# Optimization experiments

Measured on AMD Instinct MI355X. Metric: run time of the kernel, lower is better.

Reference implementation:

```python
import jax, jax.numpy as jnp
import numpy as np

NUM_LAYERS = 16
ALPHA = 1.0
EPS = 1e-20

def setup_inputs() -> dict:
    key = jax.random.key(0)
    k1, k2, k3, k4 = jax.random.split(key, 4)
    B, S, M, G = 8, 9, 8, 512
    M2 = M * M
    return {
        "dict_real": jax.random.normal(k1, (B, S, M2, G), dtype=jnp.float32),
        "dict_imag": jax.random.normal(k2, (B, S, M2, G), dtype=jnp.float32),
        "cov_real": jax.random.normal(k3, (B, S, M, M), dtype=jnp.float32),
        "cov_imag": jax.random.normal(k4, (B, S, M, M), dtype=jnp.float32),
    }

def reference(dict_real, dict_imag, cov_real, cov_imag):
    D = (dict_real + 1j * dict_imag).astype(jnp.complex64)   # (B,S,M2,G) dictionary_band
    C = (cov_real + 1j * cov_imag).astype(jnp.complex64)     # (B,S,M,M) covariance matrix
    B, S, M, _ = C.shape
    G = D.shape[-1]
    # covariance_vector = cov.transpose(2,3).reshape(B,S,M2,1)
    r = jnp.swapaxes(C, 2, 3).reshape(B, S, M * M, 1)
    Dh = jnp.conj(jnp.swapaxes(D, 2, 3))                     # (B,S,G,M2)
    DhD = jnp.matmul(Dh, D)                                  # (B,S,G,G) Hermitian PSD
    Dhr = jnp.matmul(Dh, r)                                  # (B,S,G,1)
    # initial spectrum: real part, L2-normalized over grid dim
    res = jnp.real(Dhr).astype(jnp.float32)
    res = res / (jnp.linalg.norm(res, axis=2, keepdims=True) + EPS)
    # gamma = 1 / max|eig(D^H D)|; Hermitian PSD so eigvalsh gives same max magnitude
    eig = jnp.linalg.eigvalsh(DhD)                           # (B,S,G) real
    gamma = 1.0 / jnp.max(jnp.abs(eig), axis=2, keepdims=True)        # (B,S,1)
    lam = 0.5 * jnp.max(jnp.abs(Dhr), axis=2, keepdims=True).reshape(B, S, 1)
    theta = (ALPHA * lam * gamma).reshape(B, S, 1, 1)
    g = gamma.reshape(B, S, 1, 1).astype(jnp.complex64)
    I = jnp.eye(G, dtype=jnp.complex64)
    Wt = I - g * DhD                                         # (B,S,G,G)
    Wer = g * Dhr                                            # We @ r, constant per layer

    def step(res_c, _):
        s = jnp.matmul(Wt, res_c.astype(jnp.complex64)) + Wer
        res_new = jax.nn.relu(jnp.abs(s) - theta)            # soft-shrinkage on magnitude
        return res_new, res_new

    res_final, res_all = jax.lax.scan(step, res, None, length=NUM_LAYERS)
    result_init_all = jnp.moveaxis(res_all, 0, 2)            # (B,S,L,G,1)

    def minmax_norm(x):
        lo = jnp.min(x, axis=2, keepdims=True)
        hi = jnp.max(x, axis=2, keepdims=True)
        return (x - lo) / (hi - lo + EPS)

    result_ave = minmax_norm(jnp.mean(res_final, axis=1, keepdims=True).astype(jnp.float32))
    result = minmax_norm(res_final)
    return (result, result_ave, result_init_all)
```

## Files before the change

### kernel.cpp

```cpp
#include <hip/hip_runtime.h>
#include <math.h>

#define N_SQ   7
#define INV_P  (1.0f / 256.0f)
#define EPS_F  1e-20f
#define PH     72
#define PQ     67
#define PLANE  (64 * PH)

typedef _Float16 h2    __attribute__((ext_vector_type(2)));
typedef _Float16 f16x8 __attribute__((ext_vector_type(8)));
typedef float    f32x4 __attribute__((ext_vector_type(4)));

__device__ inline float cdot2(h2 a, h2 b, float c) {
#if __has_builtin(__builtin_amdgcn_fdot2)
    return __builtin_amdgcn_fdot2(a, b, c, false);
#else
    return c + (float)a.x * (float)b.x + (float)a.y * (float)b.y;
#endif
}
__device__ inline h2 bch2(unsigned int x) { return __builtin_bit_cast(h2, x); }
__device__ inline h2 bch2f(float x)       { return __builtin_bit_cast(h2, x); }
__device__ inline float bcf(h2 x)         { return __builtin_bit_cast(float, x); }


__global__ __launch_bounds__(512, 1) void ista_main_kernel(
    const float* __restrict__ Dre, const float* __restrict__ Dim,
    const float* __restrict__ Cre, const float* __restrict__ Cim,
    float* __restrict__ out, float* __restrict__ ws)
{
    const int bs = blockIdx.x;
    const int t  = threadIdx.x;
    const int wv = t >> 6;
    const int ln = t & 63;
    const int c16 = ln & 15;
    const int qd  = ln >> 4;
    const float* __restrict__ dre = Dre + (size_t)bs * 32768;
    const float* __restrict__ dim = Dim + (size_t)bs * 32768;

    __shared__ __align__(16) float uBuf[12800];
    _Float16* ShRe  = (_Float16*)uBuf;
    _Float16* ShIm  = (_Float16*)uBuf + PLANE;
    float*    Q1    = uBuf + 4608;
    float*    resHist = uBuf + 4608;
    _Float16* sResH = (_Float16*)(uBuf + 2048);
    __shared__ __align__(16) float s_r[128];
    __shared__ float s_red[32];

    if (t < 64) {
        int i = t >> 3, j = t & 7;
        s_r[2 * t]     = Cre[bs * 64 + j * 8 + i];
        s_r[2 * t + 1] = Cim[bs * 64 + j * 8 + i];
    }

    const int tau0 = 2 * wv, tau1 = 2 * wv + 1;
    const int I0 = tau0 >> 2, J0 = tau0 & 3;
    const int I1 = tau1 >> 2, J1 = tau1 & 3;

    float Elog = 0.f, gamma = 0.f;

    auto epilogue = [&](f32x4 P0, f32x4 Qa0, f32x4 P1, f32x4 Qa1, bool first, bool last) {
        #pragma unroll
        for (int r = 0; r < 4; ++r) {
            Q1[(I0 * 16 + qd * 4 + r) * PQ + J0 * 16 + c16] = Qa0[r];
            Q1[(I1 * 16 + qd * 4 + r) * PQ + J1 * 16 + c16] = Qa1[r];
        }
        float dv = 0.f;
        if (I0 == J0) {
            #pragma unroll
            for (int r = 0; r < 4; ++r) if (qd * 4 + r == c16) dv = fmaxf(dv, fabsf(P0[r]));
        }
        if (I1 == J1) {
            #pragma unroll
            for (int r = 0; r < 4; ++r) if (qd * 4 + r == c16) dv = fmaxf(dv, fabsf(P1[r]));
        }
        for (int off = 32; off; off >>= 1) dv = fmaxf(dv, __shfl_down(dv, off, 64));
        if (ln == 0) s_red[wv] = dv;
        __syncthreads();
        float m = s_red[0];
        #pragma unroll
        for (int k = 1; k < 8; ++k) m = fmaxf(m, s_red[k]);
        Elog = first ? log2f(m) : 2.f * Elog + log2f(m);
        float ic = 1.f / m;
        float ci0[4], ci1[4];
        #pragma unroll
        for (int r = 0; r < 4; ++r) {
            ci0[r] = Qa0[r] - Q1[(J0 * 16 + c16) * PQ + I0 * 16 + qd * 4 + r];
            ci1[r] = Qa1[r] - Q1[(J1 * 16 + c16) * PQ + I1 * 16 + qd * 4 + r];
        }
        if (!last) {
            #pragma unroll
            for (int r = 0; r < 4; ++r) {
                ShRe[(I0 * 16 + qd * 4 + r) * PH + J0 * 16 + c16] = (_Float16)(P0[r] * ic);
                ShIm[(I0 * 16 + qd * 4 + r) * PH + J0 * 16 + c16] = (_Float16)(ci0[r] * ic);
                ShRe[(I1 * 16 + qd * 4 + r) * PH + J1 * 16 + c16] = (_Float16)(P1[r] * ic);
                ShIm[(I1 * 16 + qd * 4 + r) * PH + J1 * 16 + c16] = (_Float16)(ci1[r] * ic);
            }
            __syncthreads();
        } else {
            float fr = 0.f;
            #pragma unroll
            for (int r = 0; r < 4; ++r)
                fr += P0[r] * P0[r] + ci0[r] * ci0[r] + P1[r] * P1[r] + ci1[r] * ci1[r];
            fr *= ic * ic;
            for (int off = 32; off; off >>= 1) fr += __shfl_down(fr, off, 64);
            if (ln == 0) s_red[8 + wv] = fr;
            __syncthreads();
            float fsum = 0.f;
            #pragma unroll
            for (int k = 0; k < 8; ++k) fsum += s_red[8 + k];
            gamma = exp2f(-(2.f * Elog + log2f(fsum)) * INV_P);
        }
    };

    h2 du_re[32], du_im[32];
    f32x4 gP0 = {0.f, 0.f, 0.f, 0.f}, gQ0 = {0.f, 0.f, 0.f, 0.f};
    f32x4 gP1 = {0.f, 0.f, 0.f, 0.f}, gQ1 = {0.f, 0.f, 0.f, 0.f};
    {
        const int srow = t >> 4;
        const int scb  = (t & 15) * 4;
        float4 pr0, pi0, pr1, pi1;
        pr0 = *(const float4*)&dre[srow * 512 + scb];
        pi0 = *(const float4*)&dim[srow * 512 + scb];
        pr1 = *(const float4*)&dre[(srow + 32) * 512 + scb];
        pi1 = *(const float4*)&dim[(srow + 32) * 512 + scb];
        for (int ch = 0; ch < 8; ++ch) {
            *(h2*)&ShRe[srow * PH + scb]     = h2{(_Float16)pr0.x, (_Float16)pr0.y};
            *(h2*)&ShRe[srow * PH + scb + 2] = h2{(_Float16)pr0.z, (_Float16)pr0.w};
            *(h2*)&ShIm[srow * PH + scb]     = h2{(_Float16)pi0.x, (_Float16)pi0.y};
            *(h2*)&ShIm[srow * PH + scb + 2] = h2{(_Float16)pi0.z, (_Float16)pi0.w};
            *(h2*)&ShRe[(srow + 32) * PH + scb]     = h2{(_Float16)pr1.x, (_Float16)pr1.y};
            *(h2*)&ShRe[(srow + 32) * PH + scb + 2] = h2{(_Float16)pr1.z, (_Float16)pr1.w};
            *(h2*)&ShIm[(srow + 32) * PH + scb]     = h2{(_Float16)pi1.x, (_Float16)pi1.y};
            *(h2*)&ShIm[(srow + 32) * PH + scb + 2] = h2{(_Float16)pi1.z, (_Float16)pi1.w};
            if (ch < 7) {
                int gc = (ch + 1) * 64;
                pr0 = *(const float4*)&dre[srow * 512 + gc + scb];
                pi0 = *(const float4*)&dim[srow * 512 + gc + scb];
                pr1 = *(const float4*)&dre[(srow + 32) * 512 + gc + scb];
                pi1 = *(const float4*)&dim[(srow + 32) * 512 + gc + scb];
            }
            __syncthreads();
            #pragma unroll
            for (int ks = 0; ks < 64; ks += 32) {
                f16x8 arI0 = *(const f16x8*)&ShRe[(I0 * 16 + c16) * PH + ks + qd * 8];
                f16x8 aiI0 = *(const f16x8*)&ShIm[(I0 * 16 + c16) * PH + ks + qd * 8];
                f16x8 arJ0 = *(const f16x8*)&ShRe[(J0 * 16 + c16) * PH + ks + qd * 8];
                f16x8 aiJ0 = *(const f16x8*)&ShIm[(J0 * 16 + c16) * PH + ks + qd * 8];
                gP0 = __builtin_amdgcn_mfma_f32_16x16x32_f16(arI0, arJ0, gP0, 0, 0, 0);
                gP0 = __builtin_amdgcn_mfma_f32_16x16x32_f16(aiI0, aiJ0, gP0, 0, 0, 0);
                gQ0 = __builtin_amdgcn_mfma_f32_16x16x32_f16(aiI0, arJ0, gQ0, 0, 0, 0);
                f16x8 arI1 = *(const f16x8*)&ShRe[(I1 * 16 + c16) * PH + ks + qd * 8];
                f16x8 aiI1 = *(const f16x8*)&ShIm[(I1 * 16 + c16) * PH + ks + qd * 8];
                f16x8 arJ1 = *(const f16x8*)&ShRe[(J1 * 16 + c16) * PH + ks + qd * 8];
                f16x8 aiJ1 = *(const f16x8*)&ShIm[(J1 * 16 + c16) * PH + ks + qd * 8];
                gP1 = __builtin_amdgcn_mfma_f32_16x16x32_f16(arI1, arJ1, gP1, 0, 0, 0);
                gP1 = __builtin_amdgcn_mfma_f32_16x16x32_f16(aiI1, aiJ1, gP1, 0, 0, 0);
                gQ1 = __builtin_amdgcn_mfma_f32_16x16x32_f16(aiI1, arJ1, gQ1, 0, 0, 0);
            }
            if (ch == wv) {
                #pragma unroll
                for (int c = 0; c < 8; ++c) {
                    uint4 aw = *(const uint4*)&ShRe[ln * PH + 8 * c];
                    du_re[4 * c + 0] = bch2(aw.x); du_re[4 * c + 1] = bch2(aw.y);
                    du_re[4 * c + 2] = bch2(aw.z); du_re[4 * c + 3] = bch2(aw.w);
                    uint4 bw = *(const uint4*)&ShIm[ln * PH + 8 * c];
                    du_im[4 * c + 0] = bch2(bw.x); du_im[4 * c + 1] = bch2(bw.y);
                    du_im[4 * c + 2] = bch2(bw.z); du_im[4 * c + 3] = bch2(bw.w);
                }
            }
            __syncthreads();
        }
    }
    epilogue(gP0, gQ0, gP1, gQ1, true, false);

    for (int sq = 0; sq < N_SQ; ++sq) {
        f32x4 P0 = {0.f, 0.f, 0.f, 0.f}, Qa0 = {0.f, 0.f, 0.f, 0.f};
        f32x4 P1 = {0.f, 0.f, 0.f, 0.f}, Qa1 = {0.f, 0.f, 0.f, 0.f};
        #pragma unroll
        for (int ks = 0; ks < 64; ks += 32) {
            f16x8 arI0 = *(const f16x8*)&ShRe[(I0 * 16 + c16) * PH + ks + qd * 8];
            f16x8 aiI0 = *(const f16x8*)&ShIm[(I0 * 16 + c16) * PH + ks + qd * 8];
            f16x8 arJ0 = *(const f16x8*)&ShRe[(J0 * 16 + c16) * PH + ks + qd * 8];
            f16x8 aiJ0 = *(const f16x8*)&ShIm[(J0 * 16 + c16) * PH + ks + qd * 8];
            P0  = __builtin_amdgcn_mfma_f32_16x16x32_f16(arI0, arJ0, P0, 0, 0, 0);
            P0  = __builtin_amdgcn_mfma_f32_16x16x32_f16(aiI0, aiJ0, P0, 0, 0, 0);
            Qa0 = __builtin_amdgcn_mfma_f32_16x16x32_f16(aiI0, arJ0, Qa0, 0, 0, 0);
            f16x8 arI1 = *(const f16x8*)&ShRe[(I1 * 16 + c16) * PH + ks + qd * 8];
            f16x8 aiI1 = *(const f16x8*)&ShIm[(I1 * 16 + c16) * PH + ks + qd * 8];
            f16x8 arJ1 = *(const f16x8*)&ShRe[(J1 * 16 + c16) * PH + ks + qd * 8];
            f16x8 aiJ1 = *(const f16x8*)&ShIm[(J1 * 16 + c16) * PH + ks + qd * 8];
            P1  = __builtin_amdgcn_mfma_f32_16x16x32_f16(arI1, arJ1, P1, 0, 0, 0);
            P1  = __builtin_amdgcn_mfma_f32_16x16x32_f16(aiI1, aiJ1, P1, 0, 0, 0);
            Qa1 = __builtin_amdgcn_mfma_f32_16x16x32_f16(aiI1, arJ1, Qa1, 0, 0, 0);
        }
        epilogue(P0, Qa0, P1, Qa1, false, sq == N_SQ - 1);
    }

    float dhr_re, dhr_im, res_g, theta;
    h2 dV[64];
    {
        float dr0 = 0.f, dr1 = 0.f, di0 = 0.f, di1 = 0.f;
        #pragma unroll
        for (int m = 0; m < 64; ++m) {
            float ar = dre[m * 512 + t], ai = dim[m * 512 + t];
            dV[m] = h2{(_Float16)ar, (_Float16)ai};
            float rr = s_r[2 * m], ri = s_r[2 * m + 1];
            if (m & 1) { dr1 += ar * rr + ai * ri; di1 += ar * ri - ai * rr; }
            else       { dr0 += ar * rr + ai * ri; di0 += ar * ri - ai * rr; }
        }
        dhr_re = dr0 + dr1; dhr_im = di0 + di1;
        float sv = dhr_re * dhr_re;
        float mv = sqrtf(dhr_re * dhr_re + dhr_im * dhr_im);
        for (int off = 32; off; off >>= 1) {
            sv += __shfl_down(sv, off, 64);
            mv = fmaxf(mv, __shfl_down(mv, off, 64));
        }
        if (ln == 0) { s_red[16 + wv] = sv; s_red[24 + wv] = mv; }
        __syncthreads();
        float ss = 0.f, mmx = 0.f;
        #pragma unroll
        for (int k = 0; k < 8; ++k) { ss += s_red[16 + k]; mmx = fmaxf(mmx, s_red[24 + k]); }
        res_g = dhr_re / (sqrtf(ss) + EPS_F);
        theta = 0.5f * mmx * gamma;
    }

    const int resh_base = 64 * wv;
    float* const sHuMe = uBuf + 2304 + wv * 128;

    for (int l = 0; l < 16; ++l) {
        sResH[t] = (_Float16)res_g;
        float uA = 0.f, uB = 0.f, vA = 0.f, vB = 0.f;
        #pragma unroll
        for (int c = 0; c < 8; ++c) {
            uint4 rw = *(const uint4*)&sResH[resh_base + 8 * c];
            h2 r0 = bch2(rw.x), r1 = bch2(rw.y), r2 = bch2(rw.z), r3 = bch2(rw.w);
            uA = cdot2(du_re[4 * c + 0], r0, uA);  vA = cdot2(du_im[4 * c + 0], r0, vA);
            uB = cdot2(du_re[4 * c + 1], r1, uB);  vB = cdot2(du_im[4 * c + 1], r1, vB);
            uA = cdot2(du_re[4 * c + 2], r2, uA);  vA = cdot2(du_im[4 * c + 2], r2, vA);
            uB = cdot2(du_re[4 * c + 3], r3, uB);  vB = cdot2(du_im[4 * c + 3], r3, vB);
        }
        float* sUpL = uBuf + (l & 1) * 1024;
        *(float2*)&sUpL[t * 2] = make_float2(uA + uB, vA + vB);
        __syncthreads();
        float uR = 0.f, uI = 0.f;
        #pragma unroll
        for (int w8 = 0; w8 < 8; ++w8) {
            float2 p = *(const float2*)&sUpL[(w8 * 64 + ln) * 2];
            uR += p.x; uI += p.y;
        }
        h2 hu1 = h2{(_Float16)uR, (_Float16)uI};
        h2 hu2 = h2{(_Float16)uI, (_Float16)(-uR)};
        *(float2*)&sHuMe[2 * ln] = make_float2(bcf(hu1), bcf(hu2));
        float wRa = 0.f, wRb = 0.f, wIa = 0.f, wIb = 0.f;
        #pragma unroll
        for (int mm = 0; mm < 32; ++mm) {
            float4 hq = *(const float4*)&sHuMe[4 * mm];
            wRa = cdot2(dV[2 * mm],     bch2f(hq.x), wRa);
            wIa = cdot2(dV[2 * mm],     bch2f(hq.y), wIa);
            wRb = cdot2(dV[2 * mm + 1], bch2f(hq.z), wRb);
            wIb = cdot2(dV[2 * mm + 1], bch2f(hq.w), wIb);
        }
        float sre = res_g + gamma * (dhr_re - (wRa + wRb));
        float sim = gamma * (dhr_im - (wIa + wIb));
        float mag = sqrtf(sre * sre + sim * sim);
        res_g = fmaxf(mag - theta, 0.f);
        resHist[l * 512 + t] = res_g;
    }

    {
        float mn = res_g, mx = res_g;
        for (int off = 32; off; off >>= 1) {
            mn = fminf(mn, __shfl_down(mn, off, 64));
            mx = fmaxf(mx, __shfl_down(mx, off, 64));
        }
        if (ln == 0) { s_red[wv] = mn; s_red[8 + wv] = mx; }
        __syncthreads();
        float lo = s_red[0], hi = s_red[8];
        #pragma unroll
        for (int k = 1; k < 8; ++k) { lo = fminf(lo, s_red[k]); hi = fmaxf(hi, s_red[8 + k]); }
        out[bs * 512 + t] = (res_g - lo) / (hi - lo + EPS_F);
        ws[bs * 512 + t] = res_g;
    }

    {
        float* out_init = out + 40960 + (size_t)bs * 8192;
        #pragma unroll
        for (int l = 0; l < 16; ++l)
            out_init[l * 512 + t] = resHist[l * 512 + t];
    }
}

__global__ __launch_bounds__(512) void ista_ave_kernel(
    const float* __restrict__ ws, float* __restrict__ out)
{
    const int b = blockIdx.x;
    const int g = threadIdx.x;
    __shared__ float s_red[16];
    float acc = 0.f;
    #pragma unroll
    for (int s = 0; s < 9; ++s) acc += ws[(b * 9 + s) * 512 + g];
    acc *= (1.f / 9.f);
    float mn = acc, mx = acc;
    for (int off = 32; off; off >>= 1) {
        mn = fminf(mn, __shfl_down(mn, off, 64));
        mx = fmaxf(mx, __shfl_down(mx, off, 64));
    }
    if ((g & 63) == 0) { s_red[g >> 6] = mn; s_red[8 + (g >> 6)] = mx; }
    __syncthreads();
    float lo = s_red[0], hi = s_red[8];
    #pragma unroll
    for (int k = 1; k < 8; ++k) { lo = fminf(lo, s_red[k]); hi = fmaxf(hi, s_red[8 + k]); }
    out[36864 + b * 512 + g] = (acc - lo) / (hi - lo + EPS_F);
}

extern "C" void kernel_launch(void* const* d_in, const int* in_sizes, int n_in,
                              void* d_out, int out_size, void* d_ws, size_t ws_size,
                              hipStream_t stream) {
    const float* Dre = (const float*)d_in[0];
    const float* Dim = (const float*)d_in[1];
    const float* Cre = (const float*)d_in[2];
    const float* Cim = (const float*)d_in[3];
    float* out = (float*)d_out;
    float* ws  = (float*)d_ws;

    ista_main_kernel<<<72, 512, 0, stream>>>(Dre, Dim, Cre, Cim, out, ws);
    ista_ave_kernel<<<8, 512, 0, stream>>>(ws, out);
}
```

Before: 110.8 us.

## Double block to 1024 threads, one Gram tile per wave

Launches 1024 threads per block, so each of 16 waves computes one 16x16 tile of the repeated-squaring Gram products instead of two tiles per wave across 8 waves. The dictionary staging loads one row per thread instead of two. The ISTA iteration and output phases are restricted to the lower 512 threads, and reduction slots in shared memory are remapped. The aim is to halve the serial MFMA and epilogue work per wave in the squaring phase. In exchange, the 1024-thread launch bound lowers the per-thread VGPR budget, which risks spills of the large du/dV register arrays, and half the threads sit idle at barriers during the ISTA loop.

```diff
diff --git a/kernel.cpp b/kernel.cpp
--- a/kernel.cpp
+++ b/kernel.cpp
@@ -24,7 +24,7 @@
 __device__ inline float bcf(h2 x)         { return __builtin_bit_cast(float, x); }
 
 
-__global__ __launch_bounds__(512, 1) void ista_main_kernel(
+__global__ __launch_bounds__(1024, 1) void ista_main_kernel(
     const float* __restrict__ Dre, const float* __restrict__ Dim,
     const float* __restrict__ Cre, const float* __restrict__ Cim,
     float* __restrict__ out, float* __restrict__ ws)
@@ -35,6 +35,7 @@
     const int ln = t & 63;
     const int c16 = ln & 15;
     const int qd  = ln >> 4;
+    const bool lo512 = (t < 512);
     const float* __restrict__ dre = Dre + (size_t)bs * 32768;
     const float* __restrict__ dim = Dim + (size_t)bs * 32768;
 
@@ -45,7 +46,7 @@
     float*    resHist = uBuf + 4608;
     _Float16* sResH = (_Float16*)(uBuf + 2048);
     __shared__ __align__(16) float s_r[128];
-    __shared__ float s_red[32];
+    __shared__ float s_red[48];
 
     if (t < 64) {
         int i = t >> 3, j = t & 7;
@@ -53,110 +54,81 @@
         s_r[2 * t + 1] = Cim[bs * 64 + j * 8 + i];
     }
 
-    const int tau0 = 2 * wv, tau1 = 2 * wv + 1;
-    const int I0 = tau0 >> 2, J0 = tau0 & 3;
-    const int I1 = tau1 >> 2, J1 = tau1 & 3;
+    const int I = wv >> 2;
+    const int J = wv & 3;
 
     float Elog = 0.f, gamma = 0.f;
 
-    auto epilogue = [&](f32x4 P0, f32x4 Qa0, f32x4 P1, f32x4 Qa1, bool first, bool last) {
-        #pragma unroll
-        for (int r = 0; r < 4; ++r) {
-            Q1[(I0 * 16 + qd * 4 + r) * PQ + J0 * 16 + c16] = Qa0[r];
-            Q1[(I1 * 16 + qd * 4 + r) * PQ + J1 * 16 + c16] = Qa1[r];
-        }
+    auto epilogue = [&](f32x4 P, f32x4 Qa, bool first, bool last) {
+        #pragma unroll
+        for (int r = 0; r < 4; ++r)
+            Q1[(I * 16 + qd * 4 + r) * PQ + J * 16 + c16] = Qa[r];
         float dv = 0.f;
-        if (I0 == J0) {
-            #pragma unroll
-            for (int r = 0; r < 4; ++r) if (qd * 4 + r == c16) dv = fmaxf(dv, fabsf(P0[r]));
-        }
-        if (I1 == J1) {
-            #pragma unroll
-            for (int r = 0; r < 4; ++r) if (qd * 4 + r == c16) dv = fmaxf(dv, fabsf(P1[r]));
+        if (I == J) {
+            #pragma unroll
+            for (int r = 0; r < 4; ++r) if (qd * 4 + r == c16) dv = fmaxf(dv, fabsf(P[r]));
         }
         for (int off = 32; off; off >>= 1) dv = fmaxf(dv, __shfl_down(dv, off, 64));
         if (ln == 0) s_red[wv] = dv;
         __syncthreads();
         float m = s_red[0];
         #pragma unroll
-        for (int k = 1; k < 8; ++k) m = fmaxf(m, s_red[k]);
+        for (int k = 1; k < 16; ++k) m = fmaxf(m, s_red[k]);
         Elog = first ? log2f(m) : 2.f * Elog + log2f(m);
         float ic = 1.f / m;
-        float ci0[4], ci1[4];
-        #pragma unroll
-        for (int r = 0; r < 4; ++r) {
-            ci0[r] = Qa0[r] - Q1[(J0 * 16 + c16) * PQ + I0 * 16 + qd * 4 + r];
-            ci1[r] = Qa1[r] - Q1[(J1 * 16 + c16) * PQ + I1 * 16 + qd * 4 + r];
-        }
+        float ci[4];
+        #pragma unroll
+        for (int r = 0; r < 4; ++r)
+            ci[r] = Qa[r] - Q1[(J * 16 + c16) * PQ + I * 16 + qd * 4 + r];
         if (!last) {
             #pragma unroll
             for (int r = 0; r < 4; ++r) {
-                ShRe[(I0 * 16 + qd * 4 + r) * PH + J0 * 16 + c16] = (_Float16)(P0[r] * ic);
-                ShIm[(I0 * 16 + qd * 4 + r) * PH + J0 * 16 + c16] = (_Float16)(ci0[r] * ic);
-                ShRe[(I1 * 16 + qd * 4 + r) * PH + J1 * 16 + c16] = (_Float16)(P1[r] * ic);
-                ShIm[(I1 * 16 + qd * 4 + r) * PH + J1 * 16 + c16] = (_Float16)(ci1[r] * ic);
+                ShRe[(I * 16 + qd * 4 + r) * PH + J * 16 + c16] = (_Float16)(P[r] * ic);
+                ShIm[(I * 16 + qd * 4 + r) * PH + J * 16 + c16] = (_Float16)(ci[r] * ic);
             }
             __syncthreads();
         } else {
             float fr = 0.f;
             #pragma unroll
-            for (int r = 0; r < 4; ++r)
-                fr += P0[r] * P0[r] + ci0[r] * ci0[r] + P1[r] * P1[r] + ci1[r] * ci1[r];
+            for (int r = 0; r < 4; ++r) fr += P[r] * P[r] + ci[r] * ci[r];
             fr *= ic * ic;
             for (int off = 32; off; off >>= 1) fr += __shfl_down(fr, off, 64);
-            if (ln == 0) s_red[8 + wv] = fr;
+            if (ln == 0) s_red[16 + wv] = fr;
             __syncthreads();
             float fsum = 0.f;
             #pragma unroll
-            for (int k = 0; k < 8; ++k) fsum += s_red[8 + k];
+            for (int k = 0; k < 16; ++k) fsum += s_red[16 + k];
             gamma = exp2f(-(2.f * Elog + log2f(fsum)) * INV_P);
         }
     };
 
     h2 du_re[32], du_im[32];
-    f32x4 gP0 = {0.f, 0.f, 0.f, 0.f}, gQ0 = {0.f, 0.f, 0.f, 0.f};
-    f32x4 gP1 = {0.f, 0.f, 0.f, 0.f}, gQ1 = {0.f, 0.f, 0.f, 0.f};
+    f32x4 gP = {0.f, 0.f, 0.f, 0.f}, gQ = {0.f, 0.f, 0.f, 0.f};
     {
         const int srow = t >> 4;
         const int scb  = (t & 15) * 4;
-        float4 pr0, pi0, pr1, pi1;
-        pr0 = *(const float4*)&dre[srow * 512 + scb];
-        pi0 = *(const float4*)&dim[srow * 512 + scb];
-        pr1 = *(const float4*)&dre[(srow + 32) * 512 + scb];
-        pi1 = *(const float4*)&dim[(srow + 32) * 512 + scb];
+        float4 pr0 = *(const float4*)&dre[srow * 512 + scb];
+        float4 pi0 = *(const float4*)&dim[srow * 512 + scb];
         for (int ch = 0; ch < 8; ++ch) {
             *(h2*)&ShRe[srow * PH + scb]     = h2{(_Float16)pr0.x, (_Float16)pr0.y};
             *(h2*)&ShRe[srow * PH + scb + 2] = h2{(_Float16)pr0.z, (_Float16)pr0.w};
             *(h2*)&ShIm[srow * PH + scb]     = h2{(_Float16)pi0.x, (_Float16)pi0.y};
             *(h2*)&ShIm[srow * PH + scb + 2] = h2{(_Float16)pi0.z, (_Float16)pi0.w};
-            *(h2*)&ShRe[(srow + 32) * PH + scb]     = h2{(_Float16)pr1.x, (_Float16)pr1.y};
-            *(h2*)&ShRe[(srow + 32) * PH + scb + 2] = h2{(_Float16)pr1.z, (_Float16)pr1.w};
-            *(h2*)&ShIm[(srow + 32) * PH + scb]     = h2{(_Float16)pi1.x, (_Float16)pi1.y};
-            *(h2*)&ShIm[(srow + 32) * PH + scb + 2] = h2{(_Float16)pi1.z, (_Float16)pi1.w};
             if (ch < 7) {
                 int gc = (ch + 1) * 64;
                 pr0 = *(const float4*)&dre[srow * 512 + gc + scb];
                 pi0 = *(const float4*)&dim[srow * 512 + gc + scb];
-                pr1 = *(const float4*)&dre[(srow + 32) * 512 + gc + scb];
-                pi1 = *(const float4*)&dim[(srow + 32) * 512 + gc + scb];
             }
             __syncthreads();
             #pragma unroll
             for (int ks = 0; ks < 64; ks += 32) {
-                f16x8 arI0 = *(const f16x8*)&ShRe[(I0 * 16 + c16) * PH + ks + qd * 8];
-                f16x8 aiI0 = *(const f16x8*)&ShIm[(I0 * 16 + c16) * PH + ks + qd * 8];
-                f16x8 arJ0 = *(const f16x8*)&ShRe[(J0 * 16 + c16) * PH + ks + qd * 8];
-                f16x8 aiJ0 = *(const f16x8*)&ShIm[(J0 * 16 + c16) * PH + ks + qd * 8];
-                gP0 = __builtin_amdgcn_mfma_f32_16x16x32_f16(arI0, arJ0, gP0, 0, 0, 0);
-                gP0 = __builtin_amdgcn_mfma_f32_16x16x32_f16(aiI0, aiJ0, gP0, 0, 0, 0);
-                gQ0 = __builtin_amdgcn_mfma_f32_16x16x32_f16(aiI0, arJ0, gQ0, 0, 0, 0);
-                f16x8 arI1 = *(const f16x8*)&ShRe[(I1 * 16 + c16) * PH + ks + qd * 8];
-                f16x8 aiI1 = *(const f16x8*)&ShIm[(I1 * 16 + c16) * PH + ks + qd * 8];
-                f16x8 arJ1 = *(const f16x8*)&ShRe[(J1 * 16 + c16) * PH + ks + qd * 8];
-                f16x8 aiJ1 = *(const f16x8*)&ShIm[(J1 * 16 + c16) * PH + ks + qd * 8];
-                gP1 = __builtin_amdgcn_mfma_f32_16x16x32_f16(arI1, arJ1, gP1, 0, 0, 0);
-                gP1 = __builtin_amdgcn_mfma_f32_16x16x32_f16(aiI1, aiJ1, gP1, 0, 0, 0);
-                gQ1 = __builtin_amdgcn_mfma_f32_16x16x32_f16(aiI1, arJ1, gQ1, 0, 0, 0);
+                f16x8 arI = *(const f16x8*)&ShRe[(I * 16 + c16) * PH + ks + qd * 8];
+                f16x8 aiI = *(const f16x8*)&ShIm[(I * 16 + c16) * PH + ks + qd * 8];
+                f16x8 arJ = *(const f16x8*)&ShRe[(J * 16 + c16) * PH + ks + qd * 8];
+                f16x8 aiJ = *(const f16x8*)&ShIm[(J * 16 + c16) * PH + ks + qd * 8];
+                gP = __builtin_amdgcn_mfma_f32_16x16x32_f16(arI, arJ, gP, 0, 0, 0);
+                gP = __builtin_amdgcn_mfma_f32_16x16x32_f16(aiI, aiJ, gP, 0, 0, 0);
+                gQ = __builtin_amdgcn_mfma_f32_16x16x32_f16(aiI, arJ, gQ, 0, 0, 0);
             }
             if (ch == wv) {
                 #pragma unroll
@@ -172,34 +144,26 @@
             __syncthreads();
         }
     }
-    epilogue(gP0, gQ0, gP1, gQ1, true, false);
+    epilogue(gP, gQ, true, false);
 
     for (int sq = 0; sq < N_SQ; ++sq) {
-        f32x4 P0 = {0.f, 0.f, 0.f, 0.f}, Qa0 = {0.f, 0.f, 0.f, 0.f};
-        f32x4 P1 = {0.f, 0.f, 0.f, 0.f}, Qa1 = {0.f, 0.f, 0.f, 0.f};
+        f32x4 P = {0.f, 0.f, 0.f, 0.f}, Qa = {0.f, 0.f, 0.f, 0.f};
         #pragma unroll
         for (int ks = 0; ks < 64; ks += 32) {
-            f16x8 arI0 = *(const f16x8*)&ShRe[(I0 * 16 + c16) * PH + ks + qd * 8];
-            f16x8 aiI0 = *(const f16x8*)&ShIm[(I0 * 16 + c16) * PH + ks + qd * 8];
-            f16x8 arJ0 = *(const f16x8*)&ShRe[(J0 * 16 + c16) * PH + ks + qd * 8];
-            f16x8 aiJ0 = *(const f16x8*)&ShIm[(J0 * 16 + c16) * PH + ks + qd * 8];
-            P0  = __builtin_amdgcn_mfma_f32_16x16x32_f16(arI0, arJ0, P0, 0, 0, 0);
-            P0  = __builtin_amdgcn_mfma_f32_16x16x32_f16(aiI0, aiJ0, P0, 0, 0, 0);
-            Qa0 = __builtin_amdgcn_mfma_f32_16x16x32_f16(aiI0, arJ0, Qa0, 0, 0, 0);
-            f16x8 arI1 = *(const f16x8*)&ShRe[(I1 * 16 + c16) * PH + ks + qd * 8];
-            f16x8 aiI1 = *(const f16x8*)&ShIm[(I1 * 16 + c16) * PH + ks + qd * 8];
-            f16x8 arJ1 = *(const f16x8*)&ShRe[(J1 * 16 + c16) * PH + ks + qd * 8];
-            f16x8 aiJ1 = *(const f16x8*)&ShIm[(J1 * 16 + c16) * PH + ks + qd * 8];
-            P1  = __builtin_amdgcn_mfma_f32_16x16x32_f16(arI1, arJ1, P1, 0, 0, 0);
-            P1  = __builtin_amdgcn_mfma_f32_16x16x32_f16(aiI1, aiJ1, P1, 0, 0, 0);
-            Qa1 = __builtin_amdgcn_mfma_f32_16x16x32_f16(aiI1, arJ1, Qa1, 0, 0, 0);
-        }
-        epilogue(P0, Qa0, P1, Qa1, false, sq == N_SQ - 1);
-    }
-
-    float dhr_re, dhr_im, res_g, theta;
+            f16x8 arI = *(const f16x8*)&ShRe[(I * 16 + c16) * PH + ks + qd * 8];
+            f16x8 aiI = *(const f16x8*)&ShIm[(I * 16 + c16) * PH + ks + qd * 8];
+            f16x8 arJ = *(const f16x8*)&ShRe[(J * 16 + c16) * PH + ks + qd * 8];
+            f16x8 aiJ = *(const f16x8*)&ShIm[(J * 16 + c16) * PH + ks + qd * 8];
+            P  = __builtin_amdgcn_mfma_f32_16x16x32_f16(arI, arJ, P, 0, 0, 0);
+            P  = __builtin_amdgcn_mfma_f32_16x16x32_f16(aiI, aiJ, P, 0, 0, 0);
+            Qa = __builtin_amdgcn_mfma_f32_16x16x32_f16(aiI, arJ, Qa, 0, 0, 0);
+        }
+        epilogue(P, Qa, false, sq == N_SQ - 1);
+    }
+
+    float dhr_re = 0.f, dhr_im = 0.f, res_g, theta;
     h2 dV[64];
-    {
+    if (lo512) {
         float dr0 = 0.f, dr1 = 0.f, di0 = 0.f, di1 = 0.f;
         #pragma unroll
         for (int m = 0; m < 64; ++m) {
@@ -216,74 +180,82 @@
             sv += __shfl_down(sv, off, 64);
             mv = fmaxf(mv, __shfl_down(mv, off, 64));
         }
-        if (ln == 0) { s_red[16 + wv] = sv; s_red[24 + wv] = mv; }
-        __syncthreads();
+        if (ln == 0) { s_red[32 + wv] = sv; s_red[40 + wv] = mv; }
+    }
+    __syncthreads();
+    {
         float ss = 0.f, mmx = 0.f;
         #pragma unroll
-        for (int k = 0; k < 8; ++k) { ss += s_red[16 + k]; mmx = fmaxf(mmx, s_red[24 + k]); }
+        for (int k = 0; k < 8; ++k) { ss += s_red[32 + k]; mmx = fmaxf(mmx, s_red[40 + k]); }
         res_g = dhr_re / (sqrtf(ss) + EPS_F);
         theta = 0.5f * mmx * gamma;
     }
 
     const int resh_base = 64 * wv;
-    float* const sHuMe = uBuf + 2304 + wv * 128;
+    float* const sHuMe = uBuf + 2304 + (wv & 7) * 128;
 
     for (int l = 0; l < 16; ++l) {
-        sResH[t] = (_Float16)res_g;
-        float uA = 0.f, uB = 0.f, vA = 0.f, vB = 0.f;
-        #pragma unroll
-        for (int c = 0; c < 8; ++c) {
-            uint4 rw = *(const uint4*)&sResH[resh_base + 8 * c];
-            h2 r0 = bch2(rw.x), r1 = bch2(rw.y), r2 = bch2(rw.z), r3 = bch2(rw.w);
-            uA = cdot2(du_re[4 * c + 0], r0, uA);  vA = cdot2(du_im[4 * c + 0], r0, vA);
-            uB = cdot2(du_re[4 * c + 1], r1, uB);  vB = cdot2(du_im[4 * c + 1], r1, vB);
-            uA = cdot2(du_re[4 * c + 2], r2, uA);  vA = cdot2(du_im[4 * c + 2], r2, vA);
-            uB = cdot2(du_re[4 * c + 3], r3, uB);  vB = cdot2(du_im[4 * c + 3], r3, vB);
-        }
-        float* sUpL = uBuf + (l & 1) * 1024;
-        *(float2*)&sUpL[t * 2] = make_float2(uA + uB, vA + vB);
+        float upSumR = 0.f, upSumI = 0.f;
+        if (lo512) {
+            sResH[t] = (_Float16)res_g;
+            float uA = 0.f, uB = 0.f, vA = 0.f, vB = 0.f;
+            #pragma unroll
+            for (int c = 0; c < 8; ++c) {
+                uint4 rw = *(const uint4*)&sResH[resh_base + 8 * c];
+                h2 r0 = bch2(rw.x), r1 = bch2(rw.y), r2 = bch2(rw.z), r3 = bch2(rw.w);
+                uA = cdot2(du_re[4 * c + 0], r0, uA);  vA = cdot2(du_im[4 * c + 0], r0, vA);
+                uB = cdot2(du_re[4 * c + 1], r1, uB);  vB = cdot2(du_im[4 * c + 1], r1, vB);
+                uA = cdot2(du_re[4 * c + 2], r2, uA);  vA = cdot2(du_im[4 * c + 2], r2, vA);
+                uB = cdot2(du_re[4 * c + 3], r3, uB);  vB = cdot2(du_im[4 * c + 3], r3, vB);
+            }
+            upSumR = uA + uB; upSumI = vA + vB;
+            float* sUpL = uBuf + (l & 1) * 1024;
+            *(float2*)&sUpL[t * 2] = make_float2(upSumR, upSumI);
+        }
         __syncthreads();
-        float uR = 0.f, uI = 0.f;
-        #pragma unroll
-        for (int w8 = 0; w8 < 8; ++w8) {
-            float2 p = *(const float2*)&sUpL[(w8 * 64 + ln) * 2];
-            uR += p.x; uI += p.y;
-        }
-        h2 hu1 = h2{(_Float16)uR, (_Float16)uI};
-        h2 hu2 = h2{(_Float16)uI, (_Float16)(-uR)};
-        *(float2*)&sHuMe[2 * ln] = make_float2(bcf(hu1), bcf(hu2));
-        float wRa = 0.f, wRb = 0.f, wIa = 0.f, wIb = 0.f;
-        #pragma unroll
-        for (int mm = 0; mm < 32; ++mm) {
-            float4 hq = *(const float4*)&sHuMe[4 * mm];
-            wRa = cdot2(dV[2 * mm],     bch2f(hq.x), wRa);
-            wIa = cdot2(dV[2 * mm],     bch2f(hq.y), wIa);
-            wRb = cdot2(dV[2 * mm + 1], bch2f(hq.z), wRb);
-            wIb = cdot2(dV[2 * mm + 1], bch2f(hq.w), wIb);
-        }
-        float sre = res_g + gamma * (dhr_re - (wRa + wRb));
-        float sim = gamma * (dhr_im - (wIa + wIb));
-        float mag = sqrtf(sre * sre + sim * sim);
-        res_g = fmaxf(mag - theta, 0.f);
-        resHist[l * 512 + t] = res_g;
-    }
-
-    {
+        if (lo512) {
+            float* sUpL = uBuf + (l & 1) * 1024;
+            float uR = 0.f, uI = 0.f;
+            #pragma unroll
+            for (int w8 = 0; w8 < 8; ++w8) {
+                float2 p = *(const float2*)&sUpL[(w8 * 64 + ln) * 2];
+                uR += p.x; uI += p.y;
+            }
+            h2 hu1 = h2{(_Float16)uR, (_Float16)uI};
+            h2 hu2 = h2{(_Float16)uI, (_Float16)(-uR)};
+            *(float2*)&sHuMe[2 * ln] = make_float2(bcf(hu1), bcf(hu2));
+            float wRa = 0.f, wRb = 0.f, wIa = 0.f, wIb = 0.f;
+            #pragma unroll
+            for (int mm = 0; mm < 32; ++mm) {
+                float4 hq = *(const float4*)&sHuMe[4 * mm];
+                wRa = cdot2(dV[2 * mm],     bch2f(hq.x), wRa);
+                wIa = cdot2(dV[2 * mm],     bch2f(hq.y), wIa);
+                wRb = cdot2(dV[2 * mm + 1], bch2f(hq.z), wRb);
+                wIb = cdot2(dV[2 * mm + 1], bch2f(hq.w), wIb);
+            }
+            float sre = res_g + gamma * (dhr_re - (wRa + wRb));
+            float sim = gamma * (dhr_im - (wIa + wIb));
+            float mag = sqrtf(sre * sre + sim * sim);
+            res_g = fmaxf(mag - theta, 0.f);
+            resHist[l * 512 + t] = res_g;
+        }
+    }
+
+    if (lo512) {
         float mn = res_g, mx = res_g;
         for (int off = 32; off; off >>= 1) {
             mn = fminf(mn, __shfl_down(mn, off, 64));
             mx = fmaxf(mx, __shfl_down(mx, off, 64));
         }
-        if (ln == 0) { s_red[wv] = mn; s_red[8 + wv] = mx; }
-        __syncthreads();
-        float lo = s_red[0], hi = s_red[8];
-        #pragma unroll
-        for (int k = 1; k < 8; ++k) { lo = fminf(lo, s_red[k]); hi = fmaxf(hi, s_red[8 + k]); }
+        if (ln == 0) { s_red[32 + wv] = mn; s_red[40 + wv] = mx; }
+    }
+    __syncthreads();
+    if (lo512) {
+        float lo = s_red[32], hi = s_red[40];
+        #pragma unroll
+        for (int k = 1; k < 8; ++k) { lo = fminf(lo, s_red[32 + k]); hi = fmaxf(hi, s_red[40 + k]); }
         out[bs * 512 + t] = (res_g - lo) / (hi - lo + EPS_F);
         ws[bs * 512 + t] = res_g;
-    }
-
-    {
         float* out_init = out + 40960 + (size_t)bs * 8192;
         #pragma unroll
         for (int l = 0; l < 16; ++l)
@@ -324,6 +296,6 @@
     float* out = (float*)d_out;
     float* ws  = (float*)d_ws;
 
-    ista_main_kernel<<<72, 512, 0, stream>>>(Dre, Dim, Cre, Cim, out, ws);
+    ista_main_kernel<<<72, 1024, 0, stream>>>(Dre, Dim, Cre, Cim, out, ws);
     ista_ave_kernel<<<8, 512, 0, stream>>>(ws, out);
 }
```

Measured after the change: 193.2 us. 1.74x slower.
